# Performance work log

Measured on AMD Instinct MI355X. Metric: run time of the kernel, lower is better.

The kernel has to match this reference:

```python
import jax, jax.numpy as jnp
import numpy as np

N_NODES = 50000
N_EDGES = 1600000
DIM = 256
N_LAYER = 4


def setup_inputs() -> dict:
    key = jax.random.key(0)
    k1, k2, k3 = jax.random.split(key, 3)
    x = jax.random.normal(k1, (N_NODES, DIM), dtype=jnp.float32)
    edge_index = jax.random.randint(k2, (2, N_EDGES), 0, N_NODES, dtype=jnp.int64)
    # Glorot-ish scaling so activations stay O(1) across 4 layers
    W = jax.random.normal(k3, (N_LAYER, DIM, DIM), dtype=jnp.float32) / jnp.sqrt(DIM)
    b = jnp.zeros((N_LAYER, DIM), dtype=jnp.float32)
    return {"x": x, "edge_index": edge_index, "W": W, "b": b}


def reference(x, edge_index, W, b):
    N = x.shape[0]
    n_layer = W.shape[0]
    # GCNConv normalization: add self-loops, symmetric deg^{-1/2} A_hat deg^{-1/2}
    loop = jnp.arange(N, dtype=edge_index.dtype)
    src = jnp.concatenate([edge_index[0], loop])  # message source j
    dst = jnp.concatenate([edge_index[1], loop])  # message target i
    deg = jax.ops.segment_sum(jnp.ones_like(src, dtype=x.dtype), dst, num_segments=N)
    dinv = deg ** -0.5  # deg >= 1 due to self-loops
    norm = dinv[src] * dinv[dst]  # [E+N]

    def conv(h, Wl, bl):
        h = h @ Wl                                   # [N, D] dense GEMM
        msg = h[src] * norm[:, None]                 # gather + scale
        return jax.ops.segment_sum(msg, dst, num_segments=N) + bl  # scatter-add

    # norm layer is Identity (norm=None); dropout inactive in eval mode
    embeds = [x]
    hidden = conv(x, W[0], b[0])
    for i in range(1, n_layer):
        hidden = jax.nn.relu(hidden)
        embeds.append(hidden)
        hidden = conv(hidden, W[i], b[i])
    embeds.append(hidden)
    return jnp.stack(embeds)  # [n_layer+1, N, D] == embed_list (keep_init=True)
```

## Files before the change

### kernel.cpp

```cpp
#include <hip/hip_runtime.h>

#define DIM 256
#define NLAYER 4

typedef __bf16 bf16x8 __attribute__((ext_vector_type(8)));
typedef float f32x4 __attribute__((ext_vector_type(4)));
typedef float f32x2 __attribute__((ext_vector_type(2)));

__device__ __forceinline__ unsigned short f2bf(float f) {
    unsigned int u = __float_as_uint(f);
    u += 0x7fffu + ((u >> 16) & 1u);
    return (unsigned short)(u >> 16);
}

#define GLL(g, l)                                                              \
    __builtin_amdgcn_global_load_lds(                                          \
        (const __attribute__((address_space(1))) void*)(g),                    \
        (__attribute__((address_space(3))) void*)(l), 16, 0, 0)


__global__ void deg_kernel(const int* __restrict__ dst, int E, int* __restrict__ deg) {
    int e = blockIdx.x * blockDim.x + threadIdx.x;
    if (e < E) atomicAdd(&deg[dst[e]], 1);
}

__global__ void scanA_kernel(const int* __restrict__ deg, int N,
                             int* __restrict__ bsum, float* __restrict__ dinv) {
    int i = blockIdx.x * 256 + threadIdx.x;
    int v = (i < N) ? deg[i] : 0;
    if (i < N) dinv[i] = rsqrtf((float)(1 + v));
    int r = v;
#pragma unroll
    for (int o = 1; o < 64; o <<= 1) r += __shfl_xor(r, o);
    __shared__ int ws[4];
    if ((threadIdx.x & 63) == 0) ws[threadIdx.x >> 6] = r;
    __syncthreads();
    if (threadIdx.x == 0) bsum[blockIdx.x] = ws[0] + ws[1] + ws[2] + ws[3];
}

__global__ void scanB_kernel(int* __restrict__ bsum, int nb) {
    __shared__ int s[1024];
    int tid = threadIdx.x;
    int v = (tid < nb) ? bsum[tid] : 0;
    s[tid] = v;
    __syncthreads();
    for (int o = 1; o < 1024; o <<= 1) {
        int t = (tid >= o) ? s[tid - o] : 0;
        __syncthreads();
        s[tid] += t;
        __syncthreads();
    }
    if (tid < nb) bsum[tid] = s[tid] - v;
}

__global__ void scanC_kernel(int* __restrict__ deg, int N, const int* __restrict__ boff,
                             int* __restrict__ ro) {
    __shared__ int s[256];
    int tid = threadIdx.x;
    int i = blockIdx.x * 256 + tid;
    int v = (i < N) ? deg[i] : 0;
    s[tid] = v;
    __syncthreads();
    for (int o = 1; o < 256; o <<= 1) {
        int t = (tid >= o) ? s[tid - o] : 0;
        __syncthreads();
        s[tid] += t;
        __syncthreads();
    }
    int excl = s[tid] - v + boff[blockIdx.x];
    if (i < N) {
        ro[i] = excl;
        deg[i] = 0;
    }
    if (i == N - 1) ro[N] = excl + v;
}

__global__ void fill_kernel(const int* __restrict__ src, const int* __restrict__ dst, int E,
                            const int* __restrict__ ro, int* __restrict__ cursor,
                            const float* __restrict__ dinv, unsigned int* __restrict__ csr) {
    int e = blockIdx.x * blockDim.x + threadIdx.x;
    if (e < E) {
        int d = dst[e], s = src[e];
        int pos = atomicAdd(&cursor[d], 1);
        unsigned int ent = ((unsigned int)f2bf(dinv[s] * dinv[d]) << 16) | (unsigned int)s;
        csr[ro[d] + pos] = ent;
    }
}

__global__ void copy_cvt_kernel(const f32x4* __restrict__ x, f32x4* __restrict__ out,
                                ushort4* __restrict__ hb, int n4,
                                const float* __restrict__ W, unsigned short* __restrict__ Wt) {
    int gid = blockIdx.x * blockDim.x + threadIdx.x;
    int stride = gridDim.x * blockDim.x;
    for (int i = gid; i < n4; i += stride) {
        f32x4 v = x[i];
        __builtin_nontemporal_store(v, &out[i]);
        ushort4 u;
        u.x = f2bf(v[0]); u.y = f2bf(v[1]); u.z = f2bf(v[2]); u.w = f2bf(v[3]);
        hb[i] = u;
    }
    for (int i = gid; i < NLAYER * DIM * DIM; i += stride) {
        int l = i >> 16, rem = i & 65535, c = rem >> 8, k = rem & 255;
        Wt[i] = f2bf(W[(l << 16) + k * 256 + c]);
    }
}

__global__ __launch_bounds__(256, 2) void gemm_bf16(const unsigned short* __restrict__ A,
                                                    const unsigned short* __restrict__ Bt,
                                                    unsigned char* __restrict__ C, int M) {
    __shared__ unsigned short lds[16384];
    const int tid = threadIdx.x;
    const int lane = tid & 63;
    const int w = tid >> 6;
    const int brow = blockIdx.x * 128;

    f32x4 acc[8][4] = {};

    const int ar0 = tid >> 2;
    const int alu = (tid & 3) ^ ((ar0 >> 1) & 3);
    int agrow0 = brow + ar0;       if (agrow0 > M - 1) agrow0 = M - 1;
    int agrow1 = brow + ar0 + 64;  if (agrow1 > M - 1) agrow1 = M - 1;
    const unsigned short* Ag0 = A + (size_t)agrow0 * 256 + alu * 8;
    const unsigned short* Ag1 = A + (size_t)agrow1 * 256 + alu * 8;
    const int blu = (tid & 3) ^ (((tid >> 2) >> 1) & 3);
    const unsigned short* Bg = Bt + (size_t)(tid >> 2) * 256 + blu * 8;

    for (int k0 = 0; k0 < 256; k0 += 32) {
        GLL(Ag0 + k0, (char*)lds + tid * 16);
        GLL(Ag1 + k0, (char*)lds + 4096 + tid * 16);
#pragma unroll
        for (int q = 0; q < 4; ++q)
            GLL(Bg + (size_t)q * 64 * 256 + k0,
                (char*)lds + 8192 + (q * 256 + tid) * 16);
        __syncthreads();

        bf16x8 af[8], bfr[4];
#pragma unroll
        for (int mf = 0; mf < 8; ++mf) {
            int r = mf * 16 + (lane & 15);
            int su = (lane >> 4) ^ ((r >> 1) & 3);
            af[mf] = *(bf16x8*)((char*)lds + r * 64 + su * 16);
        }
#pragma unroll
        for (int nf = 0; nf < 4; ++nf) {
            int c = w * 64 + nf * 16 + (lane & 15);
            int su = (lane >> 4) ^ ((c >> 1) & 3);
            bfr[nf] = *(bf16x8*)((char*)lds + 8192 + c * 64 + su * 16);
        }
#pragma unroll
        for (int mf = 0; mf < 8; ++mf)
#pragma unroll
            for (int nf = 0; nf < 4; ++nf)
                acc[mf][nf] = __builtin_amdgcn_mfma_f32_16x16x32_bf16(af[mf], bfr[nf],
                                                                      acc[mf][nf], 0, 0, 0);
        __syncthreads();
    }

    unsigned char* cs = (unsigned char*)lds;
#pragma unroll
    for (int mf = 0; mf < 8; ++mf)
#pragma unroll
        for (int nf = 0; nf < 4; ++nf)
#pragma unroll
            for (int j = 0; j < 4; ++j) {
                int r = mf * 16 + (lane >> 4) * 4 + j;
                int c = w * 64 + nf * 16 + (lane & 15);
                int pk = __builtin_amdgcn_cvt_pk_fp8_f32(acc[mf][nf][j], acc[mf][nf][j],
                                                         0, false);
                cs[r * 256 + c] = (unsigned char)pk;
            }
    __syncthreads();
#pragma unroll
    for (int p = 0; p < 8; ++p) {
        int s = p * 256 + tid;
        int r = s >> 4;
        int o = s & 15;
        int q = o >> 2;
        int oq = o & 3;
        int grow = brow + r;
        if (grow < M)
            *(f32x4*)&C[((size_t)q * M + grow) * 64 + oq * 16] =
                *(const f32x4*)&cs[s * 16];
    }
}


__device__ __forceinline__ void accum_fp8(float4& acc, unsigned int v, float w) {
    f32x2 lo = __builtin_amdgcn_cvt_pk_f32_fp8((int)v, false);
    f32x2 hi = __builtin_amdgcn_cvt_pk_f32_fp8((int)v, true);
    acc.x += w * lo[0]; acc.y += w * lo[1];
    acc.z += w * hi[0]; acc.w += w * hi[1];
}
__device__ __forceinline__ float wof(unsigned int c) {
    return __uint_as_float(c & 0xFFFF0000u);
}

__global__ __launch_bounds__(256) void agg_kernel(const unsigned char* __restrict__ tables,
                                                  const int* __restrict__ ro,
                                                  const unsigned int* __restrict__ csr,
                                                  const float* __restrict__ dinv,
                                                  const float* __restrict__ bias,
                                                  float* __restrict__ out,
                                                  unsigned short* __restrict__ hnext,
                                                  int N, int do_relu) {
    const int q = blockIdx.y;
    const int node = blockIdx.x * 16 + (threadIdx.x >> 4);
    if (node >= N) return;
    const int gl = threadIdx.x & 15;
    const unsigned char* tab = tables + (size_t)q * N * 64;

    float4 acc;
    {
        f32x4 b4 = *(const f32x4*)&bias[q * 64 + gl * 4];
        acc = make_float4(b4[0], b4[1], b4[2], b4[3]);
    }
    float di = dinv[node];
    {
        unsigned int v = *(const unsigned int*)&tab[(size_t)node * 64 + gl * 4];
        accum_fp8(acc, v, di * di);
    }

    int e = ro[node], end = ro[node + 1];
    for (; e + 8 <= end; e += 8) {
        unsigned int c[8], v[8];
#pragma unroll
        for (int j = 0; j < 8; ++j) c[j] = csr[e + j];
#pragma unroll
        for (int j = 0; j < 8; ++j)
            v[j] = *(const unsigned int*)&tab[(size_t)(c[j] & 0xFFFFu) * 64 + gl * 4];
#pragma unroll
        for (int j = 0; j < 8; ++j) accum_fp8(acc, v[j], wof(c[j]));
    }
    for (; e + 2 <= end; e += 2) {
        unsigned int c0 = csr[e], c1 = csr[e + 1];
        unsigned int v0 = *(const unsigned int*)&tab[(size_t)(c0 & 0xFFFFu) * 64 + gl * 4];
        unsigned int v1 = *(const unsigned int*)&tab[(size_t)(c1 & 0xFFFFu) * 64 + gl * 4];
        accum_fp8(acc, v0, wof(c0));
        accum_fp8(acc, v1, wof(c1));
    }
    if (e < end) {
        unsigned int c0 = csr[e];
        unsigned int v0 = *(const unsigned int*)&tab[(size_t)(c0 & 0xFFFFu) * 64 + gl * 4];
        accum_fp8(acc, v0, wof(c0));
    }

    if (do_relu) {
        acc.x = fmaxf(acc.x, 0.f); acc.y = fmaxf(acc.y, 0.f);
        acc.z = fmaxf(acc.z, 0.f); acc.w = fmaxf(acc.w, 0.f);
    }
    f32x4 ov; ov[0] = acc.x; ov[1] = acc.y; ov[2] = acc.z; ov[3] = acc.w;
    __builtin_nontemporal_store(ov, (f32x4*)&out[(size_t)node * DIM + q * 64 + gl * 4]);
    if (hnext) {
        ushort4 u;
        u.x = f2bf(acc.x); u.y = f2bf(acc.y); u.z = f2bf(acc.z); u.w = f2bf(acc.w);
        *(ushort4*)&hnext[(size_t)node * DIM + q * 64 + gl * 4] = u;
    }
}


extern "C" void kernel_launch(void* const* d_in, const int* in_sizes, int n_in,
                              void* d_out, int out_size, void* d_ws, size_t ws_size,
                              hipStream_t stream) {
    const float* x = (const float*)d_in[0];
    const int* edge = (const int*)d_in[1];
    const float* W = (const float*)d_in[2];
    const float* b = (const float*)d_in[3];
    float* out = (float*)d_out;

    const int N = in_sizes[0] / DIM;
    const int E = in_sizes[1] / 2;
    const int* src = edge;
    const int* dst = edge + E;
    const int NB = (N + 255) / 256;

    char* ws = (char*)d_ws;
    size_t off = 0;
    auto alloc = [&](size_t bytes) {
        void* p = ws + off;
        off += (bytes + 255) & ~(size_t)255;
        return p;
    };
    int* deg = (int*)alloc((size_t)N * 4);
    int* ro = (int*)alloc((size_t)(N + 1) * 4);
    int* bsum = (int*)alloc((size_t)NB * 4);
    float* dinv = (float*)alloc((size_t)N * 4);
    unsigned int* csr = (unsigned int*)alloc((size_t)E * 4);
    unsigned char* tmp8 = (unsigned char*)alloc((size_t)N * DIM);
    unsigned short* hb = (unsigned short*)alloc((size_t)N * DIM * 2);
    unsigned short* Wt = (unsigned short*)alloc((size_t)NLAYER * DIM * DIM * 2);
    (void)ws_size;

    hipMemsetAsync(deg, 0, (size_t)N * 4, stream);
    deg_kernel<<<(E + 255) / 256, 256, 0, stream>>>(dst, E, deg);
    scanA_kernel<<<NB, 256, 0, stream>>>(deg, N, bsum, dinv);
    scanB_kernel<<<1, 1024, 0, stream>>>(bsum, NB);
    scanC_kernel<<<NB, 256, 0, stream>>>(deg, N, bsum, ro);
    fill_kernel<<<(E + 255) / 256, 256, 0, stream>>>(src, dst, E, ro, deg, dinv, csr);

    copy_cvt_kernel<<<2048, 256, 0, stream>>>((const f32x4*)x, (f32x4*)out,
                                              (ushort4*)hb, N * DIM / 4, W, Wt);

    int gemm_grid = (N + 127) / 128;
    dim3 agg_grid((N + 15) / 16, 4);
    for (int l = 0; l < NLAYER; ++l) {
        gemm_bf16<<<gemm_grid, 256, 0, stream>>>(hb, Wt + (size_t)l * DIM * DIM, tmp8, N);
        agg_kernel<<<agg_grid, 256, 0, stream>>>(
            tmp8, ro, csr, dinv, b + (size_t)l * DIM,
            out + (size_t)(l + 1) * N * DIM,
            (l < NLAYER - 1) ? hb : (unsigned short*)nullptr, N,
            (l < NLAYER - 1) ? 1 : 0);
    }
}
```

Before: 479.1 us.

## Split each node's edge list across four sub-groups per wavefront in aggregation

The aggregation kernel now gives each node a full 64-lane wavefront instead of 16 lanes. The four 16-lane sub-groups handle interleaved edges, and their partial sums are combined with xor shuffles before the store. This aims to raise memory-level parallelism for the gather and shorten the per-node dependency chain on the average degree of about 33. The cost is four times more threads, shuffle-reduction overhead, and idle lanes during the final store. The tail loop masks out-of-range edges to a zero-weight read of node 0.

Measured after the change: 560.6 us. 1.17x slower.

```diff
diff --git a/kernel.cpp b/kernel.cpp
--- a/kernel.cpp
+++ b/kernel.cpp
@@ -204,56 +204,65 @@
                                                   unsigned short* __restrict__ hnext,
                                                   int N, int do_relu) {
     const int q = blockIdx.y;
-    const int node = blockIdx.x * 16 + (threadIdx.x >> 4);
+    const int node = blockIdx.x * 4 + (threadIdx.x >> 6);
     if (node >= N) return;
-    const int gl = threadIdx.x & 15;
+    const int lane = threadIdx.x & 63;
+    const int j = lane >> 4;
+    const int gl = lane & 15;
     const unsigned char* tab = tables + (size_t)q * N * 64;
 
-    float4 acc;
-    {
+    float4 acc = make_float4(0.f, 0.f, 0.f, 0.f);
+    float di = dinv[node];
+    if (j == 0) {
         f32x4 b4 = *(const f32x4*)&bias[q * 64 + gl * 4];
         acc = make_float4(b4[0], b4[1], b4[2], b4[3]);
-    }
-    float di = dinv[node];
-    {
         unsigned int v = *(const unsigned int*)&tab[(size_t)node * 64 + gl * 4];
         accum_fp8(acc, v, di * di);
     }
 
     int e = ro[node], end = ro[node + 1];
-    for (; e + 8 <= end; e += 8) {
+    for (; e + 32 <= end; e += 32) {
         unsigned int c[8], v[8];
 #pragma unroll
-        for (int j = 0; j < 8; ++j) c[j] = csr[e + j];
-#pragma unroll
-        for (int j = 0; j < 8; ++j)
-            v[j] = *(const unsigned int*)&tab[(size_t)(c[j] & 0xFFFFu) * 64 + gl * 4];
-#pragma unroll
-        for (int j = 0; j < 8; ++j) accum_fp8(acc, v[j], wof(c[j]));
-    }
-    for (; e + 2 <= end; e += 2) {
-        unsigned int c0 = csr[e], c1 = csr[e + 1];
-        unsigned int v0 = *(const unsigned int*)&tab[(size_t)(c0 & 0xFFFFu) * 64 + gl * 4];
-        unsigned int v1 = *(const unsigned int*)&tab[(size_t)(c1 & 0xFFFFu) * 64 + gl * 4];
-        accum_fp8(acc, v0, wof(c0));
-        accum_fp8(acc, v1, wof(c1));
-    }
-    if (e < end) {
-        unsigned int c0 = csr[e];
-        unsigned int v0 = *(const unsigned int*)&tab[(size_t)(c0 & 0xFFFFu) * 64 + gl * 4];
-        accum_fp8(acc, v0, wof(c0));
-    }
-
-    if (do_relu) {
-        acc.x = fmaxf(acc.x, 0.f); acc.y = fmaxf(acc.y, 0.f);
-        acc.z = fmaxf(acc.z, 0.f); acc.w = fmaxf(acc.w, 0.f);
-    }
-    f32x4 ov; ov[0] = acc.x; ov[1] = acc.y; ov[2] = acc.z; ov[3] = acc.w;
-    __builtin_nontemporal_store(ov, (f32x4*)&out[(size_t)node * DIM + q * 64 + gl * 4]);
-    if (hnext) {
-        ushort4 u;
-        u.x = f2bf(acc.x); u.y = f2bf(acc.y); u.z = f2bf(acc.z); u.w = f2bf(acc.w);
-        *(ushort4*)&hnext[(size_t)node * DIM + q * 64 + gl * 4] = u;
+        for (int i = 0; i < 8; ++i) c[i] = csr[e + i * 4 + j];
+#pragma unroll
+        for (int i = 0; i < 8; ++i)
+            v[i] = *(const unsigned int*)&tab[(size_t)(c[i] & 0xFFFFu) * 64 + gl * 4];
+#pragma unroll
+        for (int i = 0; i < 8; ++i) accum_fp8(acc, v[i], wof(c[i]));
+    }
+    for (; e < end; e += 16) {
+        unsigned int c[4], v[4];
+#pragma unroll
+        for (int i = 0; i < 4; ++i) {
+            int idx = e + i * 4 + j;
+            c[i] = (idx < end) ? csr[idx] : 0u;
+        }
+#pragma unroll
+        for (int i = 0; i < 4; ++i)
+            v[i] = *(const unsigned int*)&tab[(size_t)(c[i] & 0xFFFFu) * 64 + gl * 4];
+#pragma unroll
+        for (int i = 0; i < 4; ++i) accum_fp8(acc, v[i], wof(c[i]));
+    }
+
+    acc.x += __shfl_xor(acc.x, 16); acc.y += __shfl_xor(acc.y, 16);
+    acc.z += __shfl_xor(acc.z, 16); acc.w += __shfl_xor(acc.w, 16);
+    acc.x += __shfl_xor(acc.x, 32); acc.y += __shfl_xor(acc.y, 32);
+    acc.z += __shfl_xor(acc.z, 32); acc.w += __shfl_xor(acc.w, 32);
+
+    if (lane < 16) {
+        if (do_relu) {
+            acc.x = fmaxf(acc.x, 0.f); acc.y = fmaxf(acc.y, 0.f);
+            acc.z = fmaxf(acc.z, 0.f); acc.w = fmaxf(acc.w, 0.f);
+        }
+        f32x4 ov; ov[0] = acc.x; ov[1] = acc.y; ov[2] = acc.z; ov[3] = acc.w;
+        __builtin_nontemporal_store(ov,
+            (f32x4*)&out[(size_t)node * DIM + q * 64 + lane * 4]);
+        if (hnext) {
+            ushort4 u;
+            u.x = f2bf(acc.x); u.y = f2bf(acc.y); u.z = f2bf(acc.z); u.w = f2bf(acc.w);
+            *(ushort4*)&hnext[(size_t)node * DIM + q * 64 + lane * 4] = u;
+        }
     }
 }
 
@@ -284,7 +293,7 @@
     int* ro = (int*)alloc((size_t)(N + 1) * 4);
     int* bsum = (int*)alloc((size_t)NB * 4);
     float* dinv = (float*)alloc((size_t)N * 4);
-    unsigned int* csr = (unsigned int*)alloc((size_t)E * 4);
+    unsigned int* csr = (unsigned int*)alloc((size_t)E * 4 + 64);
     unsigned char* tmp8 = (unsigned char*)alloc((size_t)N * DIM);
     unsigned short* hb = (unsigned short*)alloc((size_t)N * DIM * 2);
     unsigned short* Wt = (unsigned short*)alloc((size_t)NLAYER * DIM * DIM * 2);
@@ -301,7 +310,7 @@
                                               (ushort4*)hb, N * DIM / 4, W, Wt);
 
     int gemm_grid = (N + 127) / 128;
-    dim3 agg_grid((N + 15) / 16, 4);
+    dim3 agg_grid((N + 3) / 4, 4);
     for (int l = 0; l < NLAYER; ++l) {
         gemm_bf16<<<gemm_grid, 256, 0, stream>>>(hb, Wt + (size_t)l * DIM * DIM, tmp8, N);
         agg_kernel<<<agg_grid, 256, 0, stream>>>(
```
